# Kernel tuning notes

Measured on AMD Instinct MI355X. Metric: run time of the kernel, lower is better.

The kernel has to match this reference:

```python
import jax, jax.numpy as jnp
import numpy as np
from jax import lax

B, T, D, H = 32, 1024, 768, 768  # batch, seq_len, input_size, hidden_size


def setup_inputs() -> dict:
    key = jax.random.key(0)
    k1, k2, k3, k4, k5 = jax.random.split(key, 5)
    s = 1.0 / np.sqrt(H)  # torch LSTM init scale (uniform bound); use scaled normal
    return {
        "hidden": jax.random.normal(k1, (B, T, D), dtype=jnp.float32),
        "W_ih": jax.random.normal(k2, (4 * H, D), dtype=jnp.float32) * s,
        "W_hh": jax.random.normal(k3, (4 * H, H), dtype=jnp.float32) * s,
        "b_ih": jax.random.normal(k4, (4 * H,), dtype=jnp.float32) * s,
        "b_hh": jax.random.normal(k5, (4 * H,), dtype=jnp.float32) * s,
    }


def _lstm(hidden, W_ih, W_hh, b_ih, b_hh):
    # Precompute input-to-hidden gates for all timesteps: [B, T, 4H]
    xg = jnp.einsum("btd,gd->btg", hidden, W_ih) + b_ih + b_hh
    Hs = W_hh.shape[1]
    h0 = jnp.zeros((hidden.shape[0], Hs), dtype=hidden.dtype)
    c0 = jnp.zeros_like(h0)

    def step(carry, xt):
        h, c = carry
        g = xt + h @ W_hh.T                      # [B, 4H]
        i, f, gg, o = jnp.split(g, 4, axis=-1)   # torch gate order: i, f, g, o
        i = jax.nn.sigmoid(i)
        f = jax.nn.sigmoid(f)
        gg = jnp.tanh(gg)
        o = jax.nn.sigmoid(o)
        c = f * c + i * gg
        h = o * jnp.tanh(c)
        return (h, c), h

    _, ys = lax.scan(step, (h0, c0), jnp.swapaxes(xg, 0, 1))  # scan over time
    return jnp.swapaxes(ys, 0, 1)  # [B, T, H]


def reference(hidden, W_ih, W_hh, b_ih, b_hh):
    # IgLSTMRNNModule.forward: output, _ = lstm_layer(hidden); return output
    return _lstm(hidden, W_ih, W_hh, b_ih, b_hh)
```

## Files before the change

### kernel.cpp

```cpp
#include <hip/hip_runtime.h>
#include <hip/hip_fp16.h>

#define T_LEN 1024
#define B_SZ  32
#define D_IN  768
#define H_SZ  768
#define G4    3072
#define FPAD  32
#define LDA   40

typedef __attribute__((ext_vector_type(8))) short short8;
typedef __attribute__((ext_vector_type(4))) float f32x4;

__device__ __forceinline__ void split2(float x0, float x1, unsigned& hp, unsigned& lp)
{
    const unsigned u0 = __float_as_uint(x0);
    const unsigned u1 = __float_as_uint(x1);
    const unsigned h0 = u0 & 0xffff0000u, h1 = u1 & 0xffff0000u;
    hp = (h0 >> 16) | h1;
    const float l0 = x0 - __uint_as_float(h0);
    const float l1 = x1 - __uint_as_float(h1);
    lp = (__float_as_uint(l0) >> 16) | (__float_as_uint(l1) & 0xffff0000u);
}

__global__ __launch_bounds__(256, 2)
void xg_gemm(const float* __restrict__ hidden, const float* __restrict__ W_ih,
             const float* __restrict__ b_ih, const float* __restrict__ b_hh,
             __half* __restrict__ xg)
{
    __shared__ unsigned short Ah[128 * LDA];
    __shared__ unsigned short Al[128 * LDA];
    __shared__ unsigned short Bh[128 * LDA];
    __shared__ unsigned short Bl[128 * LDA];

    const int tid = threadIdx.x;
    const int n0 = blockIdx.x * 128;
    const int m0 = blockIdx.y * 128;

    const int srow = tid >> 1;
    const int skh  = (tid & 1) * 16;
    const int m = m0 + srow;
    const float* arow = hidden + ((size_t)(m & 31) * T_LEN + (m >> 5)) * D_IN;
    const float* brow = W_ih + (size_t)(n0 + srow) * D_IN;

    const int lane = tid & 63;
    const int wid  = tid >> 6;
    const int wm = (wid >> 1) * 64;
    const int wn = (wid & 1) * 64;
    const int fr = lane & 15;
    const int fk = (lane >> 4) * 8;

    f32x4 acc[4][4];
#pragma unroll
    for (int i = 0; i < 4; ++i)
#pragma unroll
        for (int j = 0; j < 4; ++j) acc[i][j] = (f32x4)0.f;

    float4 av[4], bv[4];
#pragma unroll
    for (int q = 0; q < 4; ++q) {
        av[q] = *(const float4*)(arow + skh + 4 * q);
        bv[q] = *(const float4*)(brow + skh + 4 * q);
    }

    for (int kb = 0; kb < D_IN; kb += 32) {
        __syncthreads();
        {
            const float* f = (const float*)av;
            unsigned hp[8], lp[8];
#pragma unroll
            for (int p = 0; p < 8; ++p) split2(f[2 * p], f[2 * p + 1], hp[p], lp[p]);
            *(uint4*)&Ah[srow * LDA + skh]     = make_uint4(hp[0], hp[1], hp[2], hp[3]);
            *(uint4*)&Ah[srow * LDA + skh + 8] = make_uint4(hp[4], hp[5], hp[6], hp[7]);
            *(uint4*)&Al[srow * LDA + skh]     = make_uint4(lp[0], lp[1], lp[2], lp[3]);
            *(uint4*)&Al[srow * LDA + skh + 8] = make_uint4(lp[4], lp[5], lp[6], lp[7]);
        }
        {
            const float* f = (const float*)bv;
            unsigned hp[8], lp[8];
#pragma unroll
            for (int p = 0; p < 8; ++p) split2(f[2 * p], f[2 * p + 1], hp[p], lp[p]);
            *(uint4*)&Bh[srow * LDA + skh]     = make_uint4(hp[0], hp[1], hp[2], hp[3]);
            *(uint4*)&Bh[srow * LDA + skh + 8] = make_uint4(hp[4], hp[5], hp[6], hp[7]);
            *(uint4*)&Bl[srow * LDA + skh]     = make_uint4(lp[0], lp[1], lp[2], lp[3]);
            *(uint4*)&Bl[srow * LDA + skh + 8] = make_uint4(lp[4], lp[5], lp[6], lp[7]);
        }
        __syncthreads();

        if (kb + 32 < D_IN) {
#pragma unroll
            for (int q = 0; q < 4; ++q) {
                av[q] = *(const float4*)(arow + kb + 32 + skh + 4 * q);
                bv[q] = *(const float4*)(brow + kb + 32 + skh + 4 * q);
            }
        }

        short8 afh[4], afl[4], bfh[4], bfl[4];
#pragma unroll
        for (int i = 0; i < 4; ++i) {
            afh[i] = *(const short8*)&Ah[(wm + i * 16 + fr) * LDA + fk];
            afl[i] = *(const short8*)&Al[(wm + i * 16 + fr) * LDA + fk];
            bfh[i] = *(const short8*)&Bh[(wn + i * 16 + fr) * LDA + fk];
            bfl[i] = *(const short8*)&Bl[(wn + i * 16 + fr) * LDA + fk];
        }
#pragma unroll
        for (int i = 0; i < 4; ++i)
#pragma unroll
            for (int j = 0; j < 4; ++j) {
                acc[i][j] = __builtin_amdgcn_mfma_f32_16x16x32_bf16(afh[i], bfh[j], acc[i][j], 0, 0, 0);
                acc[i][j] = __builtin_amdgcn_mfma_f32_16x16x32_bf16(afh[i], bfl[j], acc[i][j], 0, 0, 0);
                acc[i][j] = __builtin_amdgcn_mfma_f32_16x16x32_bf16(afl[i], bfh[j], acc[i][j], 0, 0, 0);
            }
    }

    const int rbase = (lane >> 4) * 4;
#pragma unroll
    for (int j = 0; j < 4; ++j) {
        const int gg = n0 + wn + j * 16 + fr;
        const int gate = gg / 768;
        const int u    = gg - gate * 768;
        const int rq   = u / 6;
        const int cj   = u - rq * 6;
        const float bias = b_ih[gg] + b_hh[gg];
        const size_t cbase = (size_t)rq * 384 + gate * 96 + cj;
#pragma unroll
        for (int i = 0; i < 4; ++i) {
#pragma unroll
            for (int rx = 0; rx < 4; ++rx) {
                const int mm = m0 + wm + i * 16 + rbase + rx;
                const int t = mm >> 5, b = mm & 31;
                const size_t addr = (((size_t)t * 2 + (b >> 4)) * 128) * 384
                                    + cbase + (b & 15) * 6;
                xg[addr] = __float2half_rn(acc[i][j][rx] + bias);
            }
        }
    }
}

__global__ void zero_cnt(unsigned* flags) {
    flags[blockIdx.x * 1024 + threadIdx.x] = 0u;
}

__device__ __forceinline__ float fast_tanh(float x) {
    const float e = __expf(-2.f * fabsf(x));
    const float r = __fdividef(1.f - e, 1.f + e);
    return copysignf(r, x);
}

__global__ void __launch_bounds__(512, 1)
lstm_rec(const __half* __restrict__ xg, const float* __restrict__ Whh,
         float* __restrict__ out, unsigned* __restrict__ flags)
{
    extern __shared__ float sm[];
    float* Wsl = sm;
    float* hsl = sm + 24 * H_SZ;
    float* G   = sm + 24 * H_SZ + 12288;

    const int tid = threadIdx.x;
    const int wg  = blockIdx.x;
    const int c   = wg & 1;
    const int r   = wg >> 1;
    const int u0  = r * 6;
    const int b0  = c * 16;

    for (int i = tid; i < 24 * 192; i += 512) {
        const int rr = i / 192;
        const int kc = (i % 192) * 4;
        const int gate = rr / 6, j = rr % 6;
        const float4 v = *(const float4*)&Whh[(size_t)(gate * H_SZ + u0 + j) * H_SZ + kc];
        *(float4*)&Wsl[rr * H_SZ + kc] = v;
    }

    const int ks     = tid & 31;
    const int tileId = tid >> 5;
    const int tr = (tileId & 3) * 6;
    const int tb = (tileId >> 2) * 4;

    const int cj = tid % 6;
    const int cb = tid / 6;
    float c_reg = 0.f;

    unsigned* myflags = flags + c * 128 * FPAD;

    __builtin_amdgcn_fence(__ATOMIC_ACQUIRE, "agent");
    __syncthreads();

    for (int t = 0; t < T_LEN; ++t) {
        float xpi = 0.f, xpf = 0.f, xpg = 0.f, xpo = 0.f;
        if (tid < 96) {
            const size_t xbase = (((size_t)t * 2 + c) * 128 + r) * 384 + tid;
            xpi = __half2float(xg[xbase + 0 * 96]);
            xpf = __half2float(xg[xbase + 1 * 96]);
            xpg = __half2float(xg[xbase + 2 * 96]);
            xpo = __half2float(xg[xbase + 3 * 96]);
        }

        if (t == 0) {
            for (int i = tid; i < 384; i += 512) G[i] = 0.f;
            __syncthreads();
        } else {
            if (tid < 128) {
                while (__hip_atomic_load(&myflags[tid * FPAD], __ATOMIC_RELAXED,
                                         __HIP_MEMORY_SCOPE_AGENT) < (unsigned)t) {
                    __builtin_amdgcn_s_sleep(2);
                }
            }
            __syncthreads();

            f32x4 hv6[6];
#pragma unroll
            for (int i = 0; i < 6; ++i) {
                const int g = i * 512 + tid;
                const int b = g / 192;
                const int k = (g - b * 192) * 4;
                const float* src = &out[((size_t)(b0 + b) * T_LEN + (t - 1)) * H_SZ + k];
                asm volatile("global_load_dwordx4 %0, %1, off sc0 sc1"
                             : "=v"(hv6[i]) : "v"(src));
            }
            asm volatile("s_waitcnt vmcnt(0)" ::: "memory");
            __builtin_amdgcn_sched_barrier(0);
#pragma unroll
            for (int i = 0; i < 6; ++i) {
                const int g = i * 512 + tid;
                const int b = g / 192;
                const int k = (g - b * 192) * 4;
                *(f32x4*)&hsl[b * H_SZ + k] = hv6[i];
            }
            __syncthreads();

            float acc[6][4];
#pragma unroll
            for (int a = 0; a < 6; ++a)
#pragma unroll
                for (int q = 0; q < 4; ++q) acc[a][q] = 0.f;

            for (int jj = 0; jj < 6; ++jj) {
                const int k = ks * 4 + jj * 128;
                float4 hv[4];
#pragma unroll
                for (int q = 0; q < 4; ++q)
                    hv[q] = *(const float4*)&hsl[(tb + q) * H_SZ + k];
#pragma unroll
                for (int a = 0; a < 6; ++a) {
                    const float4 wv = *(const float4*)&Wsl[(tr + a) * H_SZ + k];
#pragma unroll
                    for (int q = 0; q < 4; ++q) {
                        acc[a][q] = fmaf(wv.x, hv[q].x, acc[a][q]);
                        acc[a][q] = fmaf(wv.y, hv[q].y, acc[a][q]);
                        acc[a][q] = fmaf(wv.z, hv[q].z, acc[a][q]);
                        acc[a][q] = fmaf(wv.w, hv[q].w, acc[a][q]);
                    }
                }
            }
            __syncthreads();

            float* P = hsl;
#pragma unroll
            for (int a = 0; a < 6; ++a)
#pragma unroll
                for (int q = 0; q < 4; ++q)
                    P[((tr + a) * 16 + (tb + q)) * 32 + ks] = acc[a][q];
            __syncthreads();

            if (tid < 384) {
                const int oi = tid;
                float s = 0.f;
#pragma unroll
                for (int kk = 0; kk < 32; ++kk) {
                    const int k2 = (kk + oi) & 31;
                    s += P[oi * 32 + k2];
                }
                G[oi] = s;
            }
            __syncthreads();
        }

        if (tid < 96) {
            const float pi = G[(0 * 6 + cj) * 16 + cb] + xpi;
            const float pf = G[(1 * 6 + cj) * 16 + cb] + xpf;
            const float pg = G[(2 * 6 + cj) * 16 + cb] + xpg;
            const float po = G[(3 * 6 + cj) * 16 + cb] + xpo;
            const float ig = 1.f / (1.f + __expf(-pi));
            const float fg = 1.f / (1.f + __expf(-pf));
            const float gg = fast_tanh(pg);
            const float og = 1.f / (1.f + __expf(-po));
            c_reg = fg * c_reg + ig * gg;
            const float h = og * fast_tanh(c_reg);
            __hip_atomic_store(&out[((size_t)(b0 + cb) * T_LEN + t) * H_SZ + u0 + cj],
                               h, __ATOMIC_RELAXED, __HIP_MEMORY_SCOPE_AGENT);
        }
        asm volatile("s_waitcnt vmcnt(0)" ::: "memory");
        __syncthreads();

        if (tid == 0) {
            __hip_atomic_store(&myflags[r * FPAD], (unsigned)(t + 1),
                               __ATOMIC_RELAXED, __HIP_MEMORY_SCOPE_AGENT);
        }
    }
}

extern "C" void kernel_launch(void* const* d_in, const int* in_sizes, int n_in,
                              void* d_out, int out_size, void* d_ws, size_t ws_size,
                              hipStream_t stream)
{
    (void)in_sizes; (void)n_in; (void)out_size; (void)ws_size;
    const float* hidden = (const float*)d_in[0];
    const float* W_ih   = (const float*)d_in[1];
    const float* W_hh   = (const float*)d_in[2];
    const float* b_ih   = (const float*)d_in[3];
    const float* b_hh   = (const float*)d_in[4];
    float* out = (float*)d_out;

    __half* xg = (__half*)d_ws;
    unsigned* flags = (unsigned*)((char*)d_ws +
                      (size_t)T_LEN * B_SZ * G4 * sizeof(__half));

    zero_cnt<<<dim3(8), dim3(1024), 0, stream>>>(flags);
    xg_gemm<<<dim3(G4 / 128, (B_SZ * T_LEN) / 128), dim3(256), 0, stream>>>(
        hidden, W_ih, b_ih, b_hh, xg);

    const int smem = (24 * H_SZ + 12288 + 384) * (int)sizeof(float);
    (void)hipFuncSetAttribute((const void*)lstm_rec,
                              hipFuncAttributeMaxDynamicSharedMemorySize, smem);
    void* args[] = { (void*)&xg, (void*)&W_hh, (void*)&out, (void*)&flags };
    (void)hipLaunchCooperativeKernel((void*)lstm_rec, dim3(256), dim3(512),
                                     args, (unsigned)smem, stream);
}
```

Before: 5.676 ms.

## Use split-bf16 MFMA for recurrent matvec with bf16 hi/lo hidden-state exchange

Replaces the scalar FP32 FMA recurrent h·W_hh product with bf16 MFMA instructions, using a hi/lo bf16 split (three products) to approximate FP32 accuracy. Weights are pre-split into bf16 halves in padded shared memory. The hidden state is now exchanged between workgroups through a double-buffered global bf16 hi/lo buffer instead of being reread from the FP32 output. This cuts per-step ALU work and exchange bytes. It adds split arithmetic and extra stores, and drops the lo×lo term, which slightly reduces precision.

```diff
diff --git a/kernel.cpp b/kernel.cpp
--- a/kernel.cpp
+++ b/kernel.cpp
@@ -8,9 +8,14 @@
 #define G4    3072
 #define FPAD  32
 #define LDA   40
+#define HPAD  776
 
 typedef __attribute__((ext_vector_type(8))) short short8;
 typedef __attribute__((ext_vector_type(4))) float f32x4;
+typedef __attribute__((ext_vector_type(4))) unsigned u32x4;
+
+__device__ unsigned short xch_hi[2 * 2 * 16 * 768];
+__device__ unsigned short xch_lo[2 * 2 * 16 * 768];
 
 __device__ __forceinline__ void split2(float x0, float x1, unsigned& hp, unsigned& lp)
 {
@@ -151,10 +156,13 @@
 lstm_rec(const __half* __restrict__ xg, const float* __restrict__ Whh,
          float* __restrict__ out, unsigned* __restrict__ flags)
 {
-    extern __shared__ float sm[];
-    float* Wsl = sm;
-    float* hsl = sm + 24 * H_SZ;
-    float* G   = sm + 24 * H_SZ + 12288;
+    extern __shared__ char smc[];
+    unsigned short* Wh_s = (unsigned short*)smc;
+    unsigned short* Wl_s = (unsigned short*)(smc + 37248);
+    unsigned short* Hh_s = (unsigned short*)(smc + 74496);
+    unsigned short* Hl_s = (unsigned short*)(smc + 99328);
+    float*          rbuf = (float*)(smc + 124160);
+    float*          G    = (float*)(smc + 140544);
 
     const int tid = threadIdx.x;
     const int wg  = blockIdx.x;
@@ -164,17 +172,24 @@
     const int b0  = c * 16;
 
     for (int i = tid; i < 24 * 192; i += 512) {
-        const int rr = i / 192;
+        const int rr2 = i / 192;
         const int kc = (i % 192) * 4;
-        const int gate = rr / 6, j = rr % 6;
+        const int gate = rr2 / 6, j = rr2 % 6;
         const float4 v = *(const float4*)&Whh[(size_t)(gate * H_SZ + u0 + j) * H_SZ + kc];
-        *(float4*)&Wsl[rr * H_SZ + kc] = v;
-    }
-
-    const int ks     = tid & 31;
-    const int tileId = tid >> 5;
-    const int tr = (tileId & 3) * 6;
-    const int tb = (tileId >> 2) * 4;
+        unsigned h01, l01, h23, l23;
+        split2(v.x, v.y, h01, l01);
+        split2(v.z, v.w, h23, l23);
+        *(uint2*)&Wh_s[rr2 * HPAD + kc] = make_uint2(h01, h23);
+        *(uint2*)&Wl_s[rr2 * HPAD + kc] = make_uint2(l01, l23);
+    }
+
+    const int lane = tid & 63;
+    const int wv   = tid >> 6;
+    const int fr   = lane & 15;
+    const int fkb  = (lane >> 4) * 8;
+    const int rb4  = (lane >> 4) * 4;
+    const int sb   = tid >> 5;
+    const int sk0  = (tid & 31) * 24;
 
     const int cj = tid % 6;
     const int cb = tid / 6;
@@ -207,70 +222,65 @@
             }
             __syncthreads();
 
-            f32x4 hv6[6];
-#pragma unroll
-            for (int i = 0; i < 6; ++i) {
-                const int g = i * 512 + tid;
-                const int b = g / 192;
-                const int k = (g - b * 192) * 4;
-                const float* src = &out[((size_t)(b0 + b) * T_LEN + (t - 1)) * H_SZ + k];
-                asm volatile("global_load_dwordx4 %0, %1, off sc0 sc1"
-                             : "=v"(hv6[i]) : "v"(src));
-            }
-            asm volatile("s_waitcnt vmcnt(0)" ::: "memory");
-            __builtin_amdgcn_sched_barrier(0);
-#pragma unroll
-            for (int i = 0; i < 6; ++i) {
-                const int g = i * 512 + tid;
-                const int b = g / 192;
-                const int k = (g - b * 192) * 4;
-                *(f32x4*)&hsl[b * H_SZ + k] = hv6[i];
-            }
-            __syncthreads();
-
-            float acc[6][4];
-#pragma unroll
-            for (int a = 0; a < 6; ++a)
-#pragma unroll
-                for (int q = 0; q < 4; ++q) acc[a][q] = 0.f;
-
-            for (int jj = 0; jj < 6; ++jj) {
-                const int k = ks * 4 + jj * 128;
-                float4 hv[4];
-#pragma unroll
-                for (int q = 0; q < 4; ++q)
-                    hv[q] = *(const float4*)&hsl[(tb + q) * H_SZ + k];
-#pragma unroll
-                for (int a = 0; a < 6; ++a) {
-                    const float4 wv = *(const float4*)&Wsl[(tr + a) * H_SZ + k];
-#pragma unroll
-                    for (int q = 0; q < 4; ++q) {
-                        acc[a][q] = fmaf(wv.x, hv[q].x, acc[a][q]);
-                        acc[a][q] = fmaf(wv.y, hv[q].y, acc[a][q]);
-                        acc[a][q] = fmaf(wv.z, hv[q].z, acc[a][q]);
-                        acc[a][q] = fmaf(wv.w, hv[q].w, acc[a][q]);
-                    }
-                }
-            }
-            __syncthreads();
-
-            float* P = hsl;
-#pragma unroll
-            for (int a = 0; a < 6; ++a)
-#pragma unroll
-                for (int q = 0; q < 4; ++q)
-                    P[((tr + a) * 16 + (tb + q)) * 32 + ks] = acc[a][q];
+            {
+                const size_t xb = ((size_t)(c * 2 + ((t - 1) & 1)) * 16 + sb) * 768 + sk0;
+                u32x4 h0, h1, h2, l0, l1, l2;
+                asm volatile("global_load_dwordx4 %0, %1, off sc0 sc1"
+                             : "=v"(h0) : "v"(&xch_hi[xb]));
+                asm volatile("global_load_dwordx4 %0, %1, off sc0 sc1"
+                             : "=v"(h1) : "v"(&xch_hi[xb + 8]));
+                asm volatile("global_load_dwordx4 %0, %1, off sc0 sc1"
+                             : "=v"(h2) : "v"(&xch_hi[xb + 16]));
+                asm volatile("global_load_dwordx4 %0, %1, off sc0 sc1"
+                             : "=v"(l0) : "v"(&xch_lo[xb]));
+                asm volatile("global_load_dwordx4 %0, %1, off sc0 sc1"
+                             : "=v"(l1) : "v"(&xch_lo[xb + 8]));
+                asm volatile("global_load_dwordx4 %0, %1, off sc0 sc1"
+                             : "=v"(l2) : "v"(&xch_lo[xb + 16]));
+                asm volatile("s_waitcnt vmcnt(0)" ::: "memory");
+                __builtin_amdgcn_sched_barrier(0);
+                *(u32x4*)&Hh_s[sb * HPAD + sk0]      = h0;
+                *(u32x4*)&Hh_s[sb * HPAD + sk0 + 8]  = h1;
+                *(u32x4*)&Hh_s[sb * HPAD + sk0 + 16] = h2;
+                *(u32x4*)&Hl_s[sb * HPAD + sk0]      = l0;
+                *(u32x4*)&Hl_s[sb * HPAD + sk0 + 8]  = l1;
+                *(u32x4*)&Hl_s[sb * HPAD + sk0 + 16] = l2;
+            }
+            __syncthreads();
+
+            f32x4 acc0 = (f32x4)0.f, acc1 = (f32x4)0.f;
+            const int kwb = wv * 96;
+#pragma unroll
+            for (int ksd = 0; ksd < 3; ++ksd) {
+                const int ko = kwb + ksd * 32 + fkb;
+                const short8 bh  = *(const short8*)&Hh_s[fr * HPAD + ko];
+                const short8 bl  = *(const short8*)&Hl_s[fr * HPAD + ko];
+                const short8 a0h = *(const short8*)&Wh_s[fr * HPAD + ko];
+                const short8 a0l = *(const short8*)&Wl_s[fr * HPAD + ko];
+                const short8 a1h = *(const short8*)&Wh_s[(8 + fr) * HPAD + ko];
+                const short8 a1l = *(const short8*)&Wl_s[(8 + fr) * HPAD + ko];
+                acc0 = __builtin_amdgcn_mfma_f32_16x16x32_bf16(a0h, bh, acc0, 0, 0, 0);
+                acc0 = __builtin_amdgcn_mfma_f32_16x16x32_bf16(a0h, bl, acc0, 0, 0, 0);
+                acc0 = __builtin_amdgcn_mfma_f32_16x16x32_bf16(a0l, bh, acc0, 0, 0, 0);
+                acc1 = __builtin_amdgcn_mfma_f32_16x16x32_bf16(a1h, bh, acc1, 0, 0, 0);
+                acc1 = __builtin_amdgcn_mfma_f32_16x16x32_bf16(a1h, bl, acc1, 0, 0, 0);
+                acc1 = __builtin_amdgcn_mfma_f32_16x16x32_bf16(a1l, bh, acc1, 0, 0, 0);
+            }
+
+#pragma unroll
+            for (int rix = 0; rix < 4; ++rix) {
+                rbuf[wv * 512 + (rb4 + rix) * 16 + fr]        = acc0[rix];
+                rbuf[wv * 512 + (16 + rb4 + rix) * 16 + fr]   = acc1[rix];
+            }
             __syncthreads();
 
             if (tid < 384) {
-                const int oi = tid;
+                const int row = tid >> 4, colr = tid & 15;
+                const int idx = (row < 16) ? tid : ((row + 8) * 16 + colr);
                 float s = 0.f;
 #pragma unroll
-                for (int kk = 0; kk < 32; ++kk) {
-                    const int k2 = (kk + oi) & 31;
-                    s += P[oi * 32 + k2];
-                }
-                G[oi] = s;
+                for (int w = 0; w < 8; ++w) s += rbuf[w * 512 + idx];
+                G[tid] = s;
             }
             __syncthreads();
         }
@@ -286,8 +296,17 @@
             const float og = 1.f / (1.f + __expf(-po));
             c_reg = fg * c_reg + ig * gg;
             const float h = og * fast_tanh(c_reg);
-            __hip_atomic_store(&out[((size_t)(b0 + cb) * T_LEN + t) * H_SZ + u0 + cj],
-                               h, __ATOMIC_RELAXED, __HIP_MEMORY_SCOPE_AGENT);
+            out[((size_t)(b0 + cb) * T_LEN + t) * H_SZ + u0 + cj] = h;
+            const unsigned ub = __float_as_uint(h);
+            const unsigned uh = ub & 0xffff0000u;
+            const float lo = h - __uint_as_float(uh);
+            const unsigned hs = ub >> 16;
+            const unsigned ls = __float_as_uint(lo) >> 16;
+            const size_t pb = ((size_t)(c * 2 + (t & 1)) * 16 + cb) * 768 + u0 + cj;
+            asm volatile("global_store_short %0, %1, off sc0 sc1"
+                         :: "v"(&xch_hi[pb]), "v"(hs) : "memory");
+            asm volatile("global_store_short %0, %1, off sc0 sc1"
+                         :: "v"(&xch_lo[pb]), "v"(ls) : "memory");
         }
         asm volatile("s_waitcnt vmcnt(0)" ::: "memory");
         __syncthreads();
@@ -319,7 +338,7 @@
     xg_gemm<<<dim3(G4 / 128, (B_SZ * T_LEN) / 128), dim3(256), 0, stream>>>(
         hidden, W_ih, b_ih, b_hh, xg);
 
-    const int smem = (24 * H_SZ + 12288 + 384) * (int)sizeof(float);
+    const int smem = 142080;
     (void)hipFuncSetAttribute((const void*)lstm_rec,
                               hipFuncAttributeMaxDynamicSharedMemorySize, smem);
     void* args[] = { (void*)&xg, (void*)&W_hh, (void*)&out, (void*)&flags };
```

Result: faster. 5.069 ms (-10.7%).
